# Kernel optimization log

Measured on AMD Instinct MI355X. Metric: run time of the kernel, lower is better.

Reference implementation:

```python
import jax, jax.numpy as jnp
import numpy as np

B, N, E = 32, 256, 300   # batch, num hyperedges, word emb size
H, K = 256, 8            # nhidden, nhead
MARGIN = 0.2


def setup_inputs() -> dict:
    key = jax.random.key(0)
    ks = jax.random.split(key, 10)
    s_in = 1.0 / np.sqrt(E)
    s_h = 1.0 / np.sqrt(H)
    s_fc = 1.0 / np.sqrt(H * K)
    return {
        'he_anchor': jax.random.normal(ks[0], (B, N, E), jnp.float32),
        'he_pos': jax.random.normal(ks[1], (B, N, E), jnp.float32),
        'he_neg': jax.random.normal(ks[2], (B, N, E), jnp.float32),
        'W_a2h': jax.random.uniform(ks[3], (H, E), jnp.float32, -s_in, s_in),
        'b_a2h': jax.random.uniform(ks[4], (H,), jnp.float32, -s_in, s_in),
        'W_c2h': jax.random.uniform(ks[5], (H, E), jnp.float32, -s_in, s_in),
        'b_c2h': jax.random.uniform(ks[6], (H,), jnp.float32, -s_in, s_in),
        'W_att': jax.random.uniform(ks[7], (K, H), jnp.float32, -s_h, s_h),
        'b_att': jax.random.uniform(ks[8], (K,), jnp.float32, -s_h, s_h),
        'W_fc': jax.random.uniform(ks[9], (1, H * K), jnp.float32, -s_fc, s_fc),
        'b_fc': jnp.zeros((1,), jnp.float32),
    }


def _score(x, y, W_a2h, b_a2h, W_c2h, b_c2h, W_att, b_att, W_fc, b_fc):
    # a2h / c2h projections, then permute to [B, H, N]
    Aa = jnp.transpose(x @ W_a2h.T + b_a2h, (0, 2, 1))  # [B,H,N]
    Ac = jnp.transpose(y @ W_c2h.T + b_c2h, (0, 2, 1))  # [B,H,M]
    # h2att applied to the outer product Aa[b,h,n]*Ac[b,h,m]; fuse into one einsum
    logits = jnp.einsum('bhn,bhm,kh->bknm', Aa, Ac, W_att) + b_att[None, :, None, None]
    b_, k_, n_, m_ = logits.shape
    att = jax.nn.softmax(logits.reshape(b_, k_, n_ * m_), axis=-1).reshape(b_, k_, n_, m_)
    # per-head bilinear aggregation: out[b,k,h] = sum_{n,m} Aa[b,h,n]*att[b,k,n,m]*Ac[b,h,m]
    t = jnp.einsum('bhn,bknm->bkhm', Aa, att)
    out = jnp.einsum('bkhm,bhm->bkh', t, Ac)
    # torch concat order is head-major: [B, K*H]
    out = out.reshape(b_, k_ * H)
    return out @ W_fc.T + b_fc  # [B,1]


def reference(he_anchor, he_pos, he_neg, W_a2h, b_a2h, W_c2h, b_c2h, W_att, b_att, W_fc, b_fc):
    score_p = _score(he_anchor, he_pos, W_a2h, b_a2h, W_c2h, b_c2h, W_att, b_att, W_fc, b_fc)
    score_n = _score(he_anchor, he_neg, W_a2h, b_a2h, W_c2h, b_c2h, W_att, b_att, W_fc, b_fc)
    loss = jnp.mean(jax.nn.relu(score_n - score_p + MARGIN))
    return loss
```

## Files before the change

kernel.cpp:

```cpp
#include <hip/hip_runtime.h>

#define BB 32
#define NN 256
#define EE 300
#define HH 256
#define KK 8
#define MARGINF 0.2f
#define EP 320

typedef __attribute__((ext_vector_type(8))) short bf16x8;
typedef __attribute__((ext_vector_type(8))) _Float16 f16x8;
typedef __attribute__((ext_vector_type(4))) float f32x4;
typedef __attribute__((ext_vector_type(16))) float f32x16;

__device__ inline ushort f2bf(float f) {
  unsigned u = __float_as_uint(f);
  u += 0x7fffu + ((u >> 16) & 1u);
  return (ushort)(u >> 16);
}
__device__ inline unsigned pack2bf(float f0, float f1) {
  unsigned u0 = __float_as_uint(f0); u0 += 0x7fffu + ((u0 >> 16) & 1u);
  unsigned u1 = __float_as_uint(f1); u1 += 0x7fffu + ((u1 >> 16) & 1u);
  return (u0 >> 16) | (u1 & 0xffff0000u);
}

__global__ __launch_bounds__(256) void wconv_kernel(
    const float* __restrict__ Wa, const float* __restrict__ Wc,
    ushort* __restrict__ Wb, float* __restrict__ numden)
{
  if (blockIdx.x == 640) {
    const int t = threadIdx.x;
#pragma unroll
    for (int i = 0; i < 4; i++) numden[t * 4 + i] = 0.f;
    return;
  }
  const int i = blockIdx.x * 256 + threadIdx.x;
  const int e = i % EP;
  const int hw = i / EP;
  const int h = hw & 255;
  const int w = hw >> 8;
  const float* src = w ? Wc : Wa;
  Wb[i] = (e < EE) ? f2bf(src[(size_t)h * EE + e]) : (ushort)0;
}

__global__ __launch_bounds__(256, 3) void proj_kernel(
    const float* __restrict__ he_a, const float* __restrict__ he_p,
    const float* __restrict__ he_n, const ushort* __restrict__ Wb,
    const float* __restrict__ b_a2h, const float* __restrict__ b_c2h,
    _Float16* __restrict__ AT)
{
  const int z = blockIdx.y;
  const int which = z >> 5;
  const int b = z & 31;
  const int n0 = blockIdx.x * 32;
  const int tid = threadIdx.x;
  const int wv = tid >> 6;
  const int lane = tid & 63;
  const int col = lane & 15;
  const int quad = lane >> 4;

  const float* X = (which == 0 ? he_a : which == 1 ? he_p : he_n) + (size_t)b * NN * EE;
  const ushort* W = Wb + (size_t)(which == 0 ? 0 : 1) * HH * EP;
  const float* bias = (which == 0 ? b_a2h : b_c2h);

  __shared__ __align__(16) ushort sX[32][328];
  __shared__ __align__(16) _Float16 tr[32][264];

  {
    const int row = tid >> 3, seg = tid & 7;
    const float* xr = X + (size_t)(n0 + row) * EE;
#pragma unroll
    for (int q = 0; q < 10; q++) {
      const int j = seg + 8 * q;
      float4 xv = {0.f, 0.f, 0.f, 0.f};
      if (j < 75) xv = *(const float4*)&xr[4 * j];
      uint2 p; p.x = pack2bf(xv.x, xv.y); p.y = pack2bf(xv.z, xv.w);
      *(uint2*)&sX[row][4 * j] = p;
    }
  }
  __syncthreads();

  f32x4 acc[2][4];
#pragma unroll
  for (int nf = 0; nf < 2; nf++)
#pragma unroll
    for (int mb = 0; mb < 4; mb++) acc[nf][mb] = (f32x4){0.f, 0.f, 0.f, 0.f};

#pragma unroll
  for (int ks = 0; ks < 10; ks++) {
    const int off = 32 * ks + 8 * quad;
    const bf16x8 a0 = *(const bf16x8*)&sX[col][off];
    const bf16x8 a1 = *(const bf16x8*)&sX[16 + col][off];
#pragma unroll
    for (int mb = 0; mb < 4; mb++) {
      const bf16x8 w8 = *(const bf16x8*)&W[(size_t)(64 * wv + 16 * mb + col) * EP + off];
      acc[0][mb] = __builtin_amdgcn_mfma_f32_16x16x32_bf16(a0, w8, acc[0][mb], 0, 0, 0);
      acc[1][mb] = __builtin_amdgcn_mfma_f32_16x16x32_bf16(a1, w8, acc[1][mb], 0, 0, 0);
    }
  }

#pragma unroll
  for (int nf = 0; nf < 2; nf++)
#pragma unroll
    for (int mb = 0; mb < 4; mb++) {
      const float bi = bias[64 * wv + 16 * mb + col];
#pragma unroll
      for (int r = 0; r < 4; r++)
        tr[16 * nf + 4 * quad + r][64 * wv + 16 * mb + col] = (_Float16)(acc[nf][mb][r] + bi);
    }
  __syncthreads();
  {
    const int row = tid >> 3, seg = tid & 7;
    _Float16* dst = &AT[((size_t)(which * BB + b) * NN + n0 + row) * HH];
#pragma unroll
    for (int j = 0; j < 4; j++)
      *(uint4*)&dst[(seg * 4 + j) * 8] = *(const uint4*)&tr[row][(seg * 4 + j) * 8];
  }
}

__global__ __launch_bounds__(256, 1) void attn_kernel(
    const _Float16* __restrict__ AT, const float* __restrict__ Watt,
    const float* __restrict__ Wfc, float* __restrict__ numden)
{
  const int idx = blockIdx.x;
  const int q = idx >> 6;
  const int g = idx & 63;
  const int which = g >> 5;
  const int b = g & 31;
  const int tid = threadIdx.x;
  const int wv = tid >> 6;
  const int lane = tid & 63;
  const int row32 = lane & 31;
  const int half32 = lane >> 5;
  const int strip = wv & 1;
  const int mh = wv >> 1;

  const _Float16* At_a = AT + (size_t)b * NN * HH;
  const _Float16* At_c = AT + ((size_t)(1 + which) * BB + b) * NN * HH;
  const uint4* Ac_u4 = (const uint4*)At_c;

  __shared__ __align__(16) _Float16 sAc[256][264];
  __shared__ __align__(16) _Float16 wkh[8][256];
  __shared__ __align__(16) _Float16 wfh[8][256];

  const int srow = tid >> 5, scol8 = (tid & 31) * 8;
#pragma unroll
  for (int t = 0; t < 32; t++)
    *(uint4*)&sAc[8 * t + srow][scol8] = Ac_u4[(size_t)(8 * t + srow) * 32 + (tid & 31)];
#pragma unroll
  for (int kk = 0; kk < KK; kk++) {
    wkh[kk][tid] = (_Float16)Watt[kk * HH + tid];
    wfh[kk][tid] = (_Float16)Wfc[kk * HH + tid];
  }
  __syncthreads();

  const int nbase = 64 * q + 32 * strip;
  const _Float16* arow = At_a + (size_t)(nbase + row32) * HH;

#pragma unroll 1
  for (int kk = 0; kk < KK; kk++) {
    f16x8 saf[16], gaf[16];
#pragma unroll
    for (int ks = 0; ks < 16; ks++) {
      const int off = 16 * ks + 8 * half32;
      const f16x8 a = *(const f16x8*)&arow[off];
      const f16x8 w = *(const f16x8*)&wkh[kk][off];
      const f16x8 f = *(const f16x8*)&wfh[kk][off];
      saf[ks] = a * w;
      gaf[ks] = a * f;
    }

    float num = 0.f, den = 0.f;
#pragma unroll 1
    for (int mc = 0; mc < 2; mc++) {
      const int mbase = 128 * mh + 64 * mc;
      f32x16 aS0 = {0,0,0,0,0,0,0,0,0,0,0,0,0,0,0,0};
      f32x16 aS1 = {0,0,0,0,0,0,0,0,0,0,0,0,0,0,0,0};
      f32x16 aG0 = {0,0,0,0,0,0,0,0,0,0,0,0,0,0,0,0};
      f32x16 aG1 = {0,0,0,0,0,0,0,0,0,0,0,0,0,0,0,0};
#pragma unroll
      for (int ks = 0; ks < 16; ks++) {
        const int off = 16 * ks + 8 * half32;
        const f16x8 b0 = *(const f16x8*)&sAc[mbase + row32][off];
        const f16x8 b1 = *(const f16x8*)&sAc[mbase + 32 + row32][off];
        aS0 = __builtin_amdgcn_mfma_f32_32x32x16_f16(saf[ks], b0, aS0, 0, 0, 0);
        aG0 = __builtin_amdgcn_mfma_f32_32x32x16_f16(gaf[ks], b0, aG0, 0, 0, 0);
        aS1 = __builtin_amdgcn_mfma_f32_32x32x16_f16(saf[ks], b1, aS1, 0, 0, 0);
        aG1 = __builtin_amdgcn_mfma_f32_32x32x16_f16(gaf[ks], b1, aG1, 0, 0, 0);
      }
#pragma unroll
      for (int r = 0; r < 16; r++) {
        const float p0 = __expf(aS0[r]);
        den += p0; num += p0 * aG0[r];
        const float p1 = __expf(aS1[r]);
        den += p1; num += p1 * aG1[r];
      }
    }

#pragma unroll
    for (int off = 32; off >= 1; off >>= 1) {
      num += __shfl_xor(num, off);
      den += __shfl_xor(den, off);
    }
    if (lane == 0) {
      atomicAdd(&numden[(g * KK + kk) * 2 + 0], num);
      atomicAdd(&numden[(g * KK + kk) * 2 + 1], den);
    }
  }
}

__global__ __launch_bounds__(64) void loss_kernel(
    const float* __restrict__ numden, const float* __restrict__ bfc,
    float* __restrict__ out)
{
  const int tid = threadIdx.x;
  float s = bfc[0];
#pragma unroll
  for (int k = 0; k < KK; k++)
    s += numden[(tid * KK + k) * 2] / numden[(tid * KK + k) * 2 + 1];
  const float other = __shfl(s, tid + 32);
  float v = 0.f;
  if (tid < 32) v = fmaxf(other - s + MARGINF, 0.f);
#pragma unroll
  for (int off = 32; off >= 1; off >>= 1) v += __shfl_xor(v, off);
  if (tid == 0) out[0] = v * (1.0f / 32.0f);
}

extern "C" void kernel_launch(void* const* d_in, const int* in_sizes, int n_in,
                              void* d_out, int out_size, void* d_ws, size_t ws_size,
                              hipStream_t stream) {
  const float* he_a  = (const float*)d_in[0];
  const float* he_p  = (const float*)d_in[1];
  const float* he_n  = (const float*)d_in[2];
  const float* W_a2h = (const float*)d_in[3];
  const float* b_a2h = (const float*)d_in[4];
  const float* W_c2h = (const float*)d_in[5];
  const float* b_c2h = (const float*)d_in[6];
  const float* W_att = (const float*)d_in[7];
  const float* W_fc  = (const float*)d_in[9];
  const float* b_fc  = (const float*)d_in[10];

  _Float16* AT = (_Float16*)d_ws;
  ushort* Wb = (ushort*)(AT + (size_t)3 * BB * NN * HH);
  float* numden = (float*)(Wb + (size_t)2 * HH * EP);
  (void)ws_size; (void)in_sizes; (void)n_in; (void)out_size;

  wconv_kernel<<<641, 256, 0, stream>>>(W_a2h, W_c2h, Wb, numden);
  dim3 pg(8, 96);
  proj_kernel<<<pg, 256, 0, stream>>>(he_a, he_p, he_n, Wb, b_a2h, b_c2h, AT);
  attn_kernel<<<256, 256, 0, stream>>>(AT, W_att, W_fc, numden);
  loss_kernel<<<1, 64, 0, stream>>>(numden, b_fc, (float*)d_out);
}
```

Before: 148.8 us.

## Halve per-block tiles in proj and attn kernels to double grid parallelism

Result: slower. 164.6 us (+10.7%).

```diff
diff --git a/kernel.cpp b/kernel.cpp
--- a/kernel.cpp
+++ b/kernel.cpp
@@ -43,7 +43,7 @@
   Wb[i] = (e < EE) ? f2bf(src[(size_t)h * EE + e]) : (ushort)0;
 }
 
-__global__ __launch_bounds__(256, 3) void proj_kernel(
+__global__ __launch_bounds__(256, 6) void proj_kernel(
     const float* __restrict__ he_a, const float* __restrict__ he_p,
     const float* __restrict__ he_n, const ushort* __restrict__ Wb,
     const float* __restrict__ b_a2h, const float* __restrict__ b_c2h,
@@ -52,7 +52,7 @@
   const int z = blockIdx.y;
   const int which = z >> 5;
   const int b = z & 31;
-  const int n0 = blockIdx.x * 32;
+  const int n0 = blockIdx.x * 16;
   const int tid = threadIdx.x;
   const int wv = tid >> 6;
   const int lane = tid & 63;
@@ -63,15 +63,15 @@
   const ushort* W = Wb + (size_t)(which == 0 ? 0 : 1) * HH * EP;
   const float* bias = (which == 0 ? b_a2h : b_c2h);
 
-  __shared__ __align__(16) ushort sX[32][328];
-  __shared__ __align__(16) _Float16 tr[32][264];
+  __shared__ __align__(16) ushort sX[16][328];
+  __shared__ __align__(16) _Float16 tr[16][264];
 
   {
-    const int row = tid >> 3, seg = tid & 7;
+    const int row = tid >> 4, seg = tid & 15;
     const float* xr = X + (size_t)(n0 + row) * EE;
 #pragma unroll
-    for (int q = 0; q < 10; q++) {
-      const int j = seg + 8 * q;
+    for (int q = 0; q < 5; q++) {
+      const int j = seg + 16 * q;
       float4 xv = {0.f, 0.f, 0.f, 0.f};
       if (j < 75) xv = *(const float4*)&xr[4 * j];
       uint2 p; p.x = pack2bf(xv.x, xv.y); p.y = pack2bf(xv.z, xv.w);
@@ -80,50 +80,45 @@
   }
   __syncthreads();
 
-  f32x4 acc[2][4];
-#pragma unroll
-  for (int nf = 0; nf < 2; nf++)
-#pragma unroll
-    for (int mb = 0; mb < 4; mb++) acc[nf][mb] = (f32x4){0.f, 0.f, 0.f, 0.f};
+  f32x4 acc[4];
+#pragma unroll
+  for (int mb = 0; mb < 4; mb++) acc[mb] = (f32x4){0.f, 0.f, 0.f, 0.f};
 
 #pragma unroll
   for (int ks = 0; ks < 10; ks++) {
     const int off = 32 * ks + 8 * quad;
     const bf16x8 a0 = *(const bf16x8*)&sX[col][off];
-    const bf16x8 a1 = *(const bf16x8*)&sX[16 + col][off];
 #pragma unroll
     for (int mb = 0; mb < 4; mb++) {
       const bf16x8 w8 = *(const bf16x8*)&W[(size_t)(64 * wv + 16 * mb + col) * EP + off];
-      acc[0][mb] = __builtin_amdgcn_mfma_f32_16x16x32_bf16(a0, w8, acc[0][mb], 0, 0, 0);
-      acc[1][mb] = __builtin_amdgcn_mfma_f32_16x16x32_bf16(a1, w8, acc[1][mb], 0, 0, 0);
-    }
-  }
-
-#pragma unroll
-  for (int nf = 0; nf < 2; nf++)
-#pragma unroll
-    for (int mb = 0; mb < 4; mb++) {
-      const float bi = bias[64 * wv + 16 * mb + col];
-#pragma unroll
-      for (int r = 0; r < 4; r++)
-        tr[16 * nf + 4 * quad + r][64 * wv + 16 * mb + col] = (_Float16)(acc[nf][mb][r] + bi);
-    }
+      acc[mb] = __builtin_amdgcn_mfma_f32_16x16x32_bf16(a0, w8, acc[mb], 0, 0, 0);
+    }
+  }
+
+#pragma unroll
+  for (int mb = 0; mb < 4; mb++) {
+    const float bi = bias[64 * wv + 16 * mb + col];
+#pragma unroll
+    for (int r = 0; r < 4; r++)
+      tr[4 * quad + r][64 * wv + 16 * mb + col] = (_Float16)(acc[mb][r] + bi);
+  }
   __syncthreads();
   {
-    const int row = tid >> 3, seg = tid & 7;
+    const int row = tid >> 4, seg = tid & 15;
     _Float16* dst = &AT[((size_t)(which * BB + b) * NN + n0 + row) * HH];
-#pragma unroll
-    for (int j = 0; j < 4; j++)
-      *(uint4*)&dst[(seg * 4 + j) * 8] = *(const uint4*)&tr[row][(seg * 4 + j) * 8];
-  }
-}
-
-__global__ __launch_bounds__(256, 1) void attn_kernel(
+    *(uint4*)&dst[seg * 16]     = *(const uint4*)&tr[row][seg * 16];
+    *(uint4*)&dst[seg * 16 + 8] = *(const uint4*)&tr[row][seg * 16 + 8];
+  }
+}
+
+__global__ __launch_bounds__(256, 2) void attn_kernel(
     const _Float16* __restrict__ AT, const float* __restrict__ Watt,
     const float* __restrict__ Wfc, float* __restrict__ numden)
 {
   const int idx = blockIdx.x;
-  const int q = idx >> 6;
+  const int t = idx >> 6;
+  const int q = t >> 1;
+  const int mh = t & 1;
   const int g = idx & 63;
   const int which = g >> 5;
   const int b = g & 31;
@@ -133,20 +128,21 @@
   const int row32 = lane & 31;
   const int half32 = lane >> 5;
   const int strip = wv & 1;
-  const int mh = wv >> 1;
+  const int mq = wv >> 1;
 
   const _Float16* At_a = AT + (size_t)b * NN * HH;
   const _Float16* At_c = AT + ((size_t)(1 + which) * BB + b) * NN * HH;
   const uint4* Ac_u4 = (const uint4*)At_c;
 
-  __shared__ __align__(16) _Float16 sAc[256][264];
+  __shared__ __align__(16) _Float16 sAc[128][264];
   __shared__ __align__(16) _Float16 wkh[8][256];
   __shared__ __align__(16) _Float16 wfh[8][256];
 
   const int srow = tid >> 5, scol8 = (tid & 31) * 8;
 #pragma unroll
-  for (int t = 0; t < 32; t++)
-    *(uint4*)&sAc[8 * t + srow][scol8] = Ac_u4[(size_t)(8 * t + srow) * 32 + (tid & 31)];
+  for (int tt = 0; tt < 16; tt++)
+    *(uint4*)&sAc[8 * tt + srow][scol8] =
+        Ac_u4[(size_t)(128 * mh + 8 * tt + srow) * 32 + (tid & 31)];
 #pragma unroll
   for (int kk = 0; kk < KK; kk++) {
     wkh[kk][tid] = (_Float16)Watt[kk * HH + tid];
@@ -170,31 +166,28 @@
       gaf[ks] = a * f;
     }
 
+    f32x16 aS0 = {0,0,0,0,0,0,0,0,0,0,0,0,0,0,0,0};
+    f32x16 aS1 = {0,0,0,0,0,0,0,0,0,0,0,0,0,0,0,0};
+    f32x16 aG0 = {0,0,0,0,0,0,0,0,0,0,0,0,0,0,0,0};
+    f32x16 aG1 = {0,0,0,0,0,0,0,0,0,0,0,0,0,0,0,0};
+#pragma unroll
+    for (int ks = 0; ks < 16; ks++) {
+      const int off = 16 * ks + 8 * half32;
+      const f16x8 b0 = *(const f16x8*)&sAc[64 * mq + row32][off];
+      const f16x8 b1 = *(const f16x8*)&sAc[64 * mq + 32 + row32][off];
+      aS0 = __builtin_amdgcn_mfma_f32_32x32x16_f16(saf[ks], b0, aS0, 0, 0, 0);
+      aG0 = __builtin_amdgcn_mfma_f32_32x32x16_f16(gaf[ks], b0, aG0, 0, 0, 0);
+      aS1 = __builtin_amdgcn_mfma_f32_32x32x16_f16(saf[ks], b1, aS1, 0, 0, 0);
+      aG1 = __builtin_amdgcn_mfma_f32_32x32x16_f16(gaf[ks], b1, aG1, 0, 0, 0);
+    }
+
     float num = 0.f, den = 0.f;
-#pragma unroll 1
-    for (int mc = 0; mc < 2; mc++) {
-      const int mbase = 128 * mh + 64 * mc;
-      f32x16 aS0 = {0,0,0,0,0,0,0,0,0,0,0,0,0,0,0,0};
-      f32x16 aS1 = {0,0,0,0,0,0,0,0,0,0,0,0,0,0,0,0};
-      f32x16 aG0 = {0,0,0,0,0,0,0,0,0,0,0,0,0,0,0,0};
-      f32x16 aG1 = {0,0,0,0,0,0,0,0,0,0,0,0,0,0,0,0};
-#pragma unroll
-      for (int ks = 0; ks < 16; ks++) {
-        const int off = 16 * ks + 8 * half32;
-        const f16x8 b0 = *(const f16x8*)&sAc[mbase + row32][off];
-        const f16x8 b1 = *(const f16x8*)&sAc[mbase + 32 + row32][off];
-        aS0 = __builtin_amdgcn_mfma_f32_32x32x16_f16(saf[ks], b0, aS0, 0, 0, 0);
-        aG0 = __builtin_amdgcn_mfma_f32_32x32x16_f16(gaf[ks], b0, aG0, 0, 0, 0);
-        aS1 = __builtin_amdgcn_mfma_f32_32x32x16_f16(saf[ks], b1, aS1, 0, 0, 0);
-        aG1 = __builtin_amdgcn_mfma_f32_32x32x16_f16(gaf[ks], b1, aG1, 0, 0, 0);
-      }
-#pragma unroll
-      for (int r = 0; r < 16; r++) {
-        const float p0 = __expf(aS0[r]);
-        den += p0; num += p0 * aG0[r];
-        const float p1 = __expf(aS1[r]);
-        den += p1; num += p1 * aG1[r];
-      }
+#pragma unroll
+    for (int r = 0; r < 16; r++) {
+      const float p0 = __expf(aS0[r]);
+      den += p0; num += p0 * aG0[r];
+      const float p1 = __expf(aS1[r]);
+      den += p1; num += p1 * aG1[r];
     }
 
 #pragma unroll
@@ -246,8 +239,8 @@
   (void)ws_size; (void)in_sizes; (void)n_in; (void)out_size;
 
   wconv_kernel<<<641, 256, 0, stream>>>(W_a2h, W_c2h, Wb, numden);
-  dim3 pg(8, 96);
+  dim3 pg(16, 96);
   proj_kernel<<<pg, 256, 0, stream>>>(he_a, he_p, he_n, Wb, b_a2h, b_c2h, AT);
-  attn_kernel<<<256, 256, 0, stream>>>(AT, W_att, W_fc, numden);
+  attn_kernel<<<512, 256, 0, stream>>>(AT, W_att, W_fc, numden);
   loss_kernel<<<1, 64, 0, stream>>>(numden, b_fc, (float*)d_out);
 }
```

## Stage projection weights through LDS in K-chunks and split attention blocks by M-half

Applied to the files above, without the earlier changes.

Result: slower. 213.2 us (+43.3%).

```diff
diff --git a/kernel.cpp b/kernel.cpp
--- a/kernel.cpp
+++ b/kernel.cpp
@@ -43,7 +43,7 @@
   Wb[i] = (e < EE) ? f2bf(src[(size_t)h * EE + e]) : (ushort)0;
 }
 
-__global__ __launch_bounds__(256, 3) void proj_kernel(
+__global__ __launch_bounds__(256, 4) void proj_kernel(
     const float* __restrict__ he_a, const float* __restrict__ he_p,
     const float* __restrict__ he_n, const ushort* __restrict__ Wb,
     const float* __restrict__ b_a2h, const float* __restrict__ b_c2h,
@@ -63,22 +63,8 @@
   const ushort* W = Wb + (size_t)(which == 0 ? 0 : 1) * HH * EP;
   const float* bias = (which == 0 ? b_a2h : b_c2h);
 
-  __shared__ __align__(16) ushort sX[32][328];
-  __shared__ __align__(16) _Float16 tr[32][264];
-
-  {
-    const int row = tid >> 3, seg = tid & 7;
-    const float* xr = X + (size_t)(n0 + row) * EE;
-#pragma unroll
-    for (int q = 0; q < 10; q++) {
-      const int j = seg + 8 * q;
-      float4 xv = {0.f, 0.f, 0.f, 0.f};
-      if (j < 75) xv = *(const float4*)&xr[4 * j];
-      uint2 p; p.x = pack2bf(xv.x, xv.y); p.y = pack2bf(xv.z, xv.w);
-      *(uint2*)&sX[row][4 * j] = p;
-    }
-  }
-  __syncthreads();
+  __shared__ __align__(16) ushort sW[256][68];
+  __shared__ __align__(16) ushort sX[32][68];
 
   f32x4 acc[2][4];
 #pragma unroll
@@ -86,44 +72,66 @@
 #pragma unroll
     for (int mb = 0; mb < 4; mb++) acc[nf][mb] = (f32x4){0.f, 0.f, 0.f, 0.f};
 
-#pragma unroll
-  for (int ks = 0; ks < 10; ks++) {
-    const int off = 32 * ks + 8 * quad;
-    const bf16x8 a0 = *(const bf16x8*)&sX[col][off];
-    const bf16x8 a1 = *(const bf16x8*)&sX[16 + col][off];
-#pragma unroll
-    for (int mb = 0; mb < 4; mb++) {
-      const bf16x8 w8 = *(const bf16x8*)&W[(size_t)(64 * wv + 16 * mb + col) * EP + off];
-      acc[0][mb] = __builtin_amdgcn_mfma_f32_16x16x32_bf16(a0, w8, acc[0][mb], 0, 0, 0);
-      acc[1][mb] = __builtin_amdgcn_mfma_f32_16x16x32_bf16(a1, w8, acc[1][mb], 0, 0, 0);
-    }
-  }
-
-#pragma unroll
-  for (int nf = 0; nf < 2; nf++)
-#pragma unroll
-    for (int mb = 0; mb < 4; mb++) {
-      const float bi = bias[64 * wv + 16 * mb + col];
+  for (int c = 0; c < 5; c++) {
+    __syncthreads();
+    {
+      const int seg = tid & 7, rb = tid >> 3;
+      const int e0 = 64 * c + seg * 8;
+#pragma unroll
+      for (int p = 0; p < 8; p++) {
+        const int row = rb + 32 * p;
+        *(uint4*)&sW[row][seg * 8] = *(const uint4*)&W[(size_t)row * EP + e0];
+      }
+    }
+    {
+      const int s = tid & 15, rb = tid >> 4;
+#pragma unroll
+      for (int p = 0; p < 2; p++) {
+        const int row = rb + 16 * p;
+        const int e = 64 * c + 4 * s;
+        float4 xv = {0.f, 0.f, 0.f, 0.f};
+        if (e < 300) xv = *(const float4*)&X[(size_t)(n0 + row) * EE + e];
+        uint2 pk; pk.x = pack2bf(xv.x, xv.y); pk.y = pack2bf(xv.z, xv.w);
+        *(uint2*)&sX[row][4 * s] = pk;
+      }
+    }
+    __syncthreads();
+#pragma unroll
+    for (int ks = 0; ks < 2; ks++) {
+      const int off = 32 * ks + 8 * quad;
+      const bf16x8 a0 = *(const bf16x8*)&sX[col][off];
+      const bf16x8 a1 = *(const bf16x8*)&sX[16 + col][off];
+#pragma unroll
+      for (int mb = 0; mb < 4; mb++) {
+        const bf16x8 w8 = *(const bf16x8*)&sW[64 * wv + 16 * mb + col][off];
+        acc[0][mb] = __builtin_amdgcn_mfma_f32_16x16x32_bf16(a0, w8, acc[0][mb], 0, 0, 0);
+        acc[1][mb] = __builtin_amdgcn_mfma_f32_16x16x32_bf16(a1, w8, acc[1][mb], 0, 0, 0);
+      }
+    }
+  }
+
+  _Float16* dstb = &AT[(size_t)(which * BB + b) * NN * HH];
+#pragma unroll
+  for (int mb = 0; mb < 4; mb++) {
+    const int h = 64 * wv + 16 * mb + col;
+    const float bi = bias[h];
+#pragma unroll
+    for (int nf = 0; nf < 2; nf++)
 #pragma unroll
       for (int r = 0; r < 4; r++)
-        tr[16 * nf + 4 * quad + r][64 * wv + 16 * mb + col] = (_Float16)(acc[nf][mb][r] + bi);
-    }
-  __syncthreads();
-  {
-    const int row = tid >> 3, seg = tid & 7;
-    _Float16* dst = &AT[((size_t)(which * BB + b) * NN + n0 + row) * HH];
-#pragma unroll
-    for (int j = 0; j < 4; j++)
-      *(uint4*)&dst[(seg * 4 + j) * 8] = *(const uint4*)&tr[row][(seg * 4 + j) * 8];
-  }
-}
-
-__global__ __launch_bounds__(256, 1) void attn_kernel(
+        dstb[(size_t)(n0 + 16 * nf + 4 * quad + r) * HH + h] =
+            (_Float16)(acc[nf][mb][r] + bi);
+  }
+}
+
+__global__ __launch_bounds__(512, 4) void attn_kernel(
     const _Float16* __restrict__ AT, const float* __restrict__ Watt,
     const float* __restrict__ Wfc, float* __restrict__ numden)
 {
   const int idx = blockIdx.x;
-  const int q = idx >> 6;
+  const int t = idx >> 6;
+  const int q = t >> 1;
+  const int mh = t & 1;
   const int g = idx & 63;
   const int which = g >> 5;
   const int b = g & 31;
@@ -132,29 +140,33 @@
   const int lane = tid & 63;
   const int row32 = lane & 31;
   const int half32 = lane >> 5;
-  const int strip = wv & 1;
-  const int mh = wv >> 1;
+  const int strip = wv & 3;
+  const int mq = wv >> 2;
 
   const _Float16* At_a = AT + (size_t)b * NN * HH;
   const _Float16* At_c = AT + ((size_t)(1 + which) * BB + b) * NN * HH;
   const uint4* Ac_u4 = (const uint4*)At_c;
 
-  __shared__ __align__(16) _Float16 sAc[256][264];
+  __shared__ __align__(16) _Float16 sAc[128][264];
   __shared__ __align__(16) _Float16 wkh[8][256];
   __shared__ __align__(16) _Float16 wfh[8][256];
 
-  const int srow = tid >> 5, scol8 = (tid & 31) * 8;
-#pragma unroll
-  for (int t = 0; t < 32; t++)
-    *(uint4*)&sAc[8 * t + srow][scol8] = Ac_u4[(size_t)(8 * t + srow) * 32 + (tid & 31)];
-#pragma unroll
-  for (int kk = 0; kk < KK; kk++) {
-    wkh[kk][tid] = (_Float16)Watt[kk * HH + tid];
-    wfh[kk][tid] = (_Float16)Wfc[kk * HH + tid];
+#pragma unroll
+  for (int p = 0; p < 8; p++) {
+    const int u = p * 512 + tid;
+    const int row = u >> 5, c16 = u & 31;
+    *(uint4*)&sAc[row][c16 * 8] = Ac_u4[(size_t)(128 * mh + row) * 32 + c16];
+  }
+  if (tid < 256) {
+#pragma unroll
+    for (int kk = 0; kk < KK; kk++) {
+      wkh[kk][tid] = (_Float16)Watt[kk * HH + tid];
+      wfh[kk][tid] = (_Float16)Wfc[kk * HH + tid];
+    }
   }
   __syncthreads();
 
-  const int nbase = 64 * q + 32 * strip;
+  const int nbase = 128 * q + 32 * strip;
   const _Float16* arow = At_a + (size_t)(nbase + row32) * HH;
 
 #pragma unroll 1
@@ -170,31 +182,28 @@
       gaf[ks] = a * f;
     }
 
+    f32x16 aS0 = {0,0,0,0,0,0,0,0,0,0,0,0,0,0,0,0};
+    f32x16 aS1 = {0,0,0,0,0,0,0,0,0,0,0,0,0,0,0,0};
+    f32x16 aG0 = {0,0,0,0,0,0,0,0,0,0,0,0,0,0,0,0};
+    f32x16 aG1 = {0,0,0,0,0,0,0,0,0,0,0,0,0,0,0,0};
+#pragma unroll
+    for (int ks = 0; ks < 16; ks++) {
+      const int off = 16 * ks + 8 * half32;
+      const f16x8 b0 = *(const f16x8*)&sAc[64 * mq + row32][off];
+      const f16x8 b1 = *(const f16x8*)&sAc[64 * mq + 32 + row32][off];
+      aS0 = __builtin_amdgcn_mfma_f32_32x32x16_f16(saf[ks], b0, aS0, 0, 0, 0);
+      aG0 = __builtin_amdgcn_mfma_f32_32x32x16_f16(gaf[ks], b0, aG0, 0, 0, 0);
+      aS1 = __builtin_amdgcn_mfma_f32_32x32x16_f16(saf[ks], b1, aS1, 0, 0, 0);
+      aG1 = __builtin_amdgcn_mfma_f32_32x32x16_f16(gaf[ks], b1, aG1, 0, 0, 0);
+    }
+
     float num = 0.f, den = 0.f;
-#pragma unroll 1
-    for (int mc = 0; mc < 2; mc++) {
-      const int mbase = 128 * mh + 64 * mc;
-      f32x16 aS0 = {0,0,0,0,0,0,0,0,0,0,0,0,0,0,0,0};
-      f32x16 aS1 = {0,0,0,0,0,0,0,0,0,0,0,0,0,0,0,0};
-      f32x16 aG0 = {0,0,0,0,0,0,0,0,0,0,0,0,0,0,0,0};
-      f32x16 aG1 = {0,0,0,0,0,0,0,0,0,0,0,0,0,0,0,0};
-#pragma unroll
-      for (int ks = 0; ks < 16; ks++) {
-        const int off = 16 * ks + 8 * half32;
-        const f16x8 b0 = *(const f16x8*)&sAc[mbase + row32][off];
-        const f16x8 b1 = *(const f16x8*)&sAc[mbase + 32 + row32][off];
-        aS0 = __builtin_amdgcn_mfma_f32_32x32x16_f16(saf[ks], b0, aS0, 0, 0, 0);
-        aG0 = __builtin_amdgcn_mfma_f32_32x32x16_f16(gaf[ks], b0, aG0, 0, 0, 0);
-        aS1 = __builtin_amdgcn_mfma_f32_32x32x16_f16(saf[ks], b1, aS1, 0, 0, 0);
-        aG1 = __builtin_amdgcn_mfma_f32_32x32x16_f16(gaf[ks], b1, aG1, 0, 0, 0);
-      }
-#pragma unroll
-      for (int r = 0; r < 16; r++) {
-        const float p0 = __expf(aS0[r]);
-        den += p0; num += p0 * aG0[r];
-        const float p1 = __expf(aS1[r]);
-        den += p1; num += p1 * aG1[r];
-      }
+#pragma unroll
+    for (int r = 0; r < 16; r++) {
+      const float p0 = __expf(aS0[r]);
+      den += p0; num += p0 * aG0[r];
+      const float p1 = __expf(aS1[r]);
+      den += p1; num += p1 * aG1[r];
     }
 
 #pragma unroll
@@ -248,6 +257,6 @@
   wconv_kernel<<<641, 256, 0, stream>>>(W_a2h, W_c2h, Wb, numden);
   dim3 pg(8, 96);
   proj_kernel<<<pg, 256, 0, stream>>>(he_a, he_p, he_n, Wb, b_a2h, b_c2h, AT);
-  attn_kernel<<<256, 256, 0, stream>>>(AT, W_att, W_fc, numden);
+  attn_kernel<<<256, 512, 0, stream>>>(AT, W_att, W_fc, numden);
   loss_kernel<<<1, 64, 0, stream>>>(numden, b_fc, (float*)d_out);
 }
```
